# Kernel optimization log

Hardware: AMD Instinct MI355X
Metric: run time of the kernel (lower is better)

## Reference

```python
import jax, jax.numpy as jnp
import numpy as np
from jax import lax

B, T, I, H = 128, 512, 300, 256


def setup_inputs() -> dict:
    key = jax.random.key(0)
    ks = jax.random.split(key, 10)
    k = 1.0 / np.sqrt(H)
    u = lambda kk, shape: jax.random.uniform(kk, shape, jnp.float32, -k, k)
    return {
        "x": jax.random.normal(ks[0], (B, T, I), jnp.float32),
        "W_ih_f": u(ks[1], (4 * H, I)),
        "W_hh_f": u(ks[2], (4 * H, H)),
        "b_f": u(ks[3], (4 * H,)),
        "W_ih_b": u(ks[4], (4 * H, I)),
        "W_hh_b": u(ks[5], (4 * H, H)),
        "b_b": u(ks[6], (4 * H,)),
        "W_lin": u(ks[7], (2, 2 * H)),
        "b_lin": u(ks[8], (2,)),
    }


def _lstm_dir(x, W_ih, W_hh, b, reverse):
    # Precompute input projections for all timesteps: [B, T, 4H]
    xp = jnp.einsum("bti,gi->btg", x, W_ih) + b
    if reverse:
        xp = xp[:, ::-1]
    h0 = jnp.zeros((x.shape[0], H), x.dtype)
    c0 = jnp.zeros((x.shape[0], H), x.dtype)

    def step(carry, xt):
        h, c = carry
        g = xt + h @ W_hh.T  # [B, 4H]
        i_g, f_g, g_g, o_g = jnp.split(g, 4, axis=-1)  # torch gate order i,f,g,o
        i_g = jax.nn.sigmoid(i_g)
        f_g = jax.nn.sigmoid(f_g)
        g_g = jnp.tanh(g_g)
        o_g = jax.nn.sigmoid(o_g)
        c = f_g * c + i_g * g_g
        h = o_g * jnp.tanh(c)
        return (h, c), h

    _, hs = lax.scan(step, (h0, c0), jnp.swapaxes(xp, 0, 1))  # [T, B, H]
    hs = jnp.swapaxes(hs, 0, 1)  # [B, T, H]
    if reverse:
        hs = hs[:, ::-1]
    return hs


def reference(x, W_ih_f, W_hh_f, b_f, W_ih_b, W_hh_b, b_b, W_lin, b_lin):
    hf = _lstm_dir(x, W_ih_f, W_hh_f, b_f, reverse=False)  # [B, T, H]
    hb = _lstm_dir(x, W_ih_b, W_hh_b, b_b, reverse=True)   # [B, T, H]
    last = jnp.concatenate([hf[:, -1], hb[:, -1]], axis=-1)  # [B, 2H]
    return last @ W_lin.T + b_lin  # [B, 2]
```

## Files before the change

### kernel.cpp

```cpp
#include <hip/hip_runtime.h>
#include <cstdint>
#include <cstddef>

typedef _Float16 half2v __attribute__((ext_vector_type(2)));
typedef _Float16 half4v __attribute__((ext_vector_type(4)));
typedef _Float16 half8v __attribute__((ext_vector_type(8)));
typedef float f32x4 __attribute__((ext_vector_type(4)));

#if __has_builtin(__builtin_amdgcn_fdot2)
#define FDOT2(a, b, c) __builtin_amdgcn_fdot2((a), (b), (c), false)
#else
static __device__ __forceinline__ float fdot2_fb(half2v a, half2v b, float c) {
    return c + (float)a[0] * (float)b[0] + (float)a[1] * (float)b[1];
}
#define FDOT2(a, b, c) fdot2_fb((a), (b), (c))
#endif

__device__ __forceinline__ float sigm(float x) { return 1.0f / (1.0f + __expf(-x)); }
__device__ __forceinline__ float tanh_(float x) { return 1.0f - 2.0f / (__expf(2.0f * x) + 1.0f); }

#define BB 128
#define TT 512
#define II 300
#define HH 256
#define GG 1024

__global__ __launch_bounds__(256, 3) void gemm_xp(
    const float* __restrict__ X, const float* __restrict__ W,
    const float* __restrict__ bias, _Float16* __restrict__ XP)
{
    __shared__ _Float16 As[128 * 32];
    __shared__ _Float16 Bs[128 * 32];

    const int t = threadIdx.x;
    const int m0 = blockIdx.y * 128;
    const int n0 = blockIdx.x * 128;
    const int kpos = t & 7;
    const int rbase = t >> 3;
    const int lane = t & 63;
    const int wv = t >> 6;
    const int mq = (wv >> 1) * 4;
    const int nq = (wv & 1) * 4;

    f32x4 acc[4][4];
#pragma unroll
    for (int i = 0; i < 4; ++i)
#pragma unroll
        for (int j = 0; j < 4; ++j) acc[i][j] = f32x4{0.f, 0.f, 0.f, 0.f};

    for (int kc = 0; kc < 320; kc += 32) {
        __syncthreads();
        const int k0 = kc + kpos * 4;
#pragma unroll
        for (int rr = 0; rr < 4; ++rr) {
            const int row = rbase + rr * 32;
            float4 va = {0.f, 0.f, 0.f, 0.f}, vb = {0.f, 0.f, 0.f, 0.f};
            if (k0 < 300) {
                va = *(const float4*)(X + (size_t)(m0 + row) * II + k0);
                vb = *(const float4*)(W + (size_t)(n0 + row) * II + k0);
            }
            const int idx = (row >> 4) * 512 + (kpos >> 1) * 128 + (row & 15) * 8 + (kpos & 1) * 4;
            half4v ha = {(_Float16)va.x, (_Float16)va.y, (_Float16)va.z, (_Float16)va.w};
            half4v hb = {(_Float16)vb.x, (_Float16)vb.y, (_Float16)vb.z, (_Float16)vb.w};
            *(half4v*)(&As[idx]) = ha;
            *(half4v*)(&Bs[idx]) = hb;
        }
        __syncthreads();

        half8v af[4], bf[4];
#pragma unroll
        for (int i = 0; i < 4; ++i) {
            af[i] = *(const half8v*)(&As[(mq + i) * 512 + (lane >> 4) * 128 + (lane & 15) * 8]);
            bf[i] = *(const half8v*)(&Bs[(nq + i) * 512 + (lane >> 4) * 128 + (lane & 15) * 8]);
        }
#pragma unroll
        for (int i = 0; i < 4; ++i)
#pragma unroll
            for (int j = 0; j < 4; ++j)
                acc[i][j] = __builtin_amdgcn_mfma_f32_16x16x32_f16(af[i], bf[j], acc[i][j], 0, 0, 0);
    }

#pragma unroll
    for (int j = 0; j < 4; ++j) {
        const int n = n0 + (nq + j) * 16 + (lane & 15);
        const float bv = bias[n];
#pragma unroll
        for (int i = 0; i < 4; ++i) {
#pragma unroll
            for (int r = 0; r < 4; ++r) {
                const int m = m0 + (mq + i) * 16 + (lane >> 4) * 4 + r;
                XP[(size_t)m * GG + n] = (_Float16)(acc[i][j][r] + bv);
            }
        }
    }
}

__global__ __launch_bounds__(512, 2) void lstm_fwd(
    const float* __restrict__ Whh, const _Float16* __restrict__ XP,
    float* __restrict__ HF)
{
    __shared__ _Float16 wlds[8 * GG * 8];
    __shared__ float glds[GG];
    __shared__ __align__(16) _Float16 hlds[HH];

    const int t = threadIdx.x;
    const int b = blockIdx.x;
    const int r1 = t + 512;

    half2v w0[96], w1[96];
#pragma unroll
    for (int i = 0; i < 48; ++i) {
        float4 v = *(const float4*)(Whh + (size_t)t * HH + i * 4);
        w0[2 * i]     = half2v{(_Float16)v.x, (_Float16)v.y};
        w0[2 * i + 1] = half2v{(_Float16)v.z, (_Float16)v.w};
    }
#pragma unroll
    for (int i = 0; i < 48; ++i) {
        float4 v = *(const float4*)(Whh + (size_t)r1 * HH + i * 4);
        w1[2 * i]     = half2v{(_Float16)v.x, (_Float16)v.y};
        w1[2 * i + 1] = half2v{(_Float16)v.z, (_Float16)v.w};
    }
#pragma unroll
    for (int grp = 0; grp < 8; ++grp) {
        float4 a  = *(const float4*)(Whh + (size_t)t * HH + 192 + grp * 8);
        float4 c4 = *(const float4*)(Whh + (size_t)t * HH + 192 + grp * 8 + 4);
        half8v hv = {(_Float16)a.x, (_Float16)a.y, (_Float16)a.z, (_Float16)a.w,
                     (_Float16)c4.x, (_Float16)c4.y, (_Float16)c4.z, (_Float16)c4.w};
        *(half8v*)(&wlds[grp * (GG * 8) + t * 8]) = hv;
        float4 a2 = *(const float4*)(Whh + (size_t)r1 * HH + 192 + grp * 8);
        float4 c2 = *(const float4*)(Whh + (size_t)r1 * HH + 192 + grp * 8 + 4);
        half8v hv2 = {(_Float16)a2.x, (_Float16)a2.y, (_Float16)a2.z, (_Float16)a2.w,
                      (_Float16)c2.x, (_Float16)c2.y, (_Float16)c2.z, (_Float16)c2.w};
        *(half8v*)(&wlds[grp * (GG * 8) + r1 * 8]) = hv2;
    }
    if (t < HH) hlds[t] = (_Float16)0.f;
    float c = 0.0f;
    __syncthreads();

    const _Float16* xp_b = XP + (size_t)b * TT * GG;
    _Float16 x0 = xp_b[t];
    _Float16 x1 = xp_b[r1];

    for (int ts = 0; ts < TT; ++ts) {
        const _Float16* xp_n = xp_b + ((ts < TT - 1) ? GG : 0);
        const _Float16 nx0 = xp_n[t];
        const _Float16 nx1 = xp_n[r1];

        float a0 = 0.f, a1 = 0.f;
#pragma unroll
        for (int cq = 0; cq < 24; ++cq) {
            half8v hv = *(const half8v*)(&hlds[cq * 8]);
            half2v h0 = __builtin_shufflevector(hv, hv, 0, 1);
            half2v h1 = __builtin_shufflevector(hv, hv, 2, 3);
            half2v h2 = __builtin_shufflevector(hv, hv, 4, 5);
            half2v h3 = __builtin_shufflevector(hv, hv, 6, 7);
            a0 = FDOT2(h0, w0[cq * 4 + 0], a0);
            a1 = FDOT2(h0, w1[cq * 4 + 0], a1);
            a0 = FDOT2(h1, w0[cq * 4 + 1], a0);
            a1 = FDOT2(h1, w1[cq * 4 + 1], a1);
            a0 = FDOT2(h2, w0[cq * 4 + 2], a0);
            a1 = FDOT2(h2, w1[cq * 4 + 2], a1);
            a0 = FDOT2(h3, w0[cq * 4 + 3], a0);
            a1 = FDOT2(h3, w1[cq * 4 + 3], a1);
        }
#define LDS_W_STEP(W_IDX, I0, I1)                                          \
        {                                                                  \
            half2v hp  = __builtin_shufflevector(hv, hv, I0, I1);          \
            half2v wap = __builtin_shufflevector(wa, wa, I0, I1);          \
            half2v wbp = __builtin_shufflevector(wb, wb, I0, I1);          \
            a0 = FDOT2(hp, wap, a0);                                       \
            a1 = FDOT2(hp, wbp, a1);                                       \
        }
#pragma unroll
        for (int grp = 0; grp < 8; ++grp) {
            half8v hv = *(const half8v*)(&hlds[192 + grp * 8]);
            half8v wa = *(const half8v*)(&wlds[grp * (GG * 8) + t * 8]);
            half8v wb = *(const half8v*)(&wlds[grp * (GG * 8) + r1 * 8]);
            LDS_W_STEP(0, 0, 1)
            LDS_W_STEP(1, 2, 3)
            LDS_W_STEP(2, 4, 5)
            LDS_W_STEP(3, 6, 7)
        }
#undef LDS_W_STEP
        const float o0 = a0 + (float)x0;
        const float o1 = a1 + (float)x1;
        glds[t] = o0;
        glds[t + 512] = o1;
        __syncthreads();
        const float p0 = glds[t ^ 256];
        const float p1 = glds[(t ^ 256) + 512];
        const float gi = (t < 256) ? o0 : p0;
        const float gg = (t < 256) ? o1 : p1;
        const float gf = (t < 256) ? p0 : o0;
        const float go = (t < 256) ? p1 : o1;
        c = sigm(gf) * c + sigm(gi) * tanh_(gg);
        const float h = sigm(go) * tanh_(c);
        if (t < HH) {
            hlds[t] = (_Float16)h;
            if (ts == TT - 1) HF[(size_t)b * HH + t] = h;
        }
        __syncthreads();

        x0 = nx0;
        x1 = nx1;
        xp_b = xp_n;
    }
}

__global__ __launch_bounds__(256) void lstm_bwd(
    const float* __restrict__ X, const float* __restrict__ Wih,
    const float* __restrict__ bb, float* __restrict__ HB)
{
    __shared__ float xs[II];
    const int b = blockIdx.x, t = threadIdx.x;
    const float* xrow = X + ((size_t)b * TT + (TT - 1)) * II;
    if (t < 75) *(float4*)(&xs[t * 4]) = *(const float4*)(xrow + t * 4);
    __syncthreads();
    if (t < HH) {
        float ai = 0.f, ag = 0.f, ao = 0.f;
        const float4* wi = (const float4*)(Wih + (size_t)t * II);
        const float4* wg = (const float4*)(Wih + (size_t)(t + 512) * II);
        const float4* wo = (const float4*)(Wih + (size_t)(t + 768) * II);
        for (int k4 = 0; k4 < 75; ++k4) {
            float4 xv = *(const float4*)(&xs[k4 * 4]);
            float4 a = wi[k4], g4 = wg[k4], o4 = wo[k4];
            ai += xv.x * a.x + xv.y * a.y + xv.z * a.z + xv.w * a.w;
            ag += xv.x * g4.x + xv.y * g4.y + xv.z * g4.z + xv.w * g4.w;
            ao += xv.x * o4.x + xv.y * o4.y + xv.z * o4.z + xv.w * o4.w;
        }
        ai += bb[t];
        ag += bb[t + 512];
        ao += bb[t + 768];
        const float cg = sigm(ai) * tanh_(ag);
        HB[(size_t)b * HH + t] = sigm(ao) * tanh_(cg);
    }
}

__global__ __launch_bounds__(256) void final_k(
    const float* __restrict__ HF, const float* __restrict__ HB,
    const float* __restrict__ Wlin, const float* __restrict__ blin,
    float* __restrict__ OUT)
{
    const int t = threadIdx.x;
    const int b = t >> 1, jj = t & 1;
    float acc = blin[jj];
    const float* wf = Wlin + jj * 512;
    const float* wb = Wlin + jj * 512 + 256;
    const float* hf = HF + (size_t)b * HH;
    const float* hb = HB + (size_t)b * HH;
    for (int k = 0; k < HH; k += 4) {
        float4 h4 = *(const float4*)(hf + k);
        float4 w4 = *(const float4*)(wf + k);
        float4 g4 = *(const float4*)(hb + k);
        float4 v4 = *(const float4*)(wb + k);
        acc += h4.x * w4.x + h4.y * w4.y + h4.z * w4.z + h4.w * w4.w;
        acc += g4.x * v4.x + g4.y * v4.y + g4.z * v4.z + g4.w * v4.w;
    }
    OUT[b * 2 + jj] = acc;
}

extern "C" void kernel_launch(void* const* d_in, const int* in_sizes, int n_in,
                              void* d_out, int out_size, void* d_ws, size_t ws_size,
                              hipStream_t stream)
{
    const float* x = (const float*)d_in[0];
    const float* Wihf = (const float*)d_in[1];
    const float* Whhf = (const float*)d_in[2];
    const float* bf = (const float*)d_in[3];
    const float* Wihb = (const float*)d_in[4];
    const float* Whhb = (const float*)d_in[5];
    const float* bbv = (const float*)d_in[6];
    const float* Wlin = (const float*)d_in[7];
    const float* blin = (const float*)d_in[8];
    float* out = (float*)d_out;
    (void)Whhb; (void)in_sizes; (void)n_in; (void)out_size; (void)ws_size;

    _Float16* xp = (_Float16*)d_ws;
    float* hf = (float*)((char*)d_ws + (size_t)BB * TT * GG * 2);
    float* hb = hf + (size_t)BB * HH;

    lstm_bwd<<<BB, 256, 0, stream>>>(x, Wihb, bbv, hb);
    gemm_xp<<<dim3(GG / 128, (BB * TT) / 128), 256, 0, stream>>>(x, Wihf, bf, xp);
    lstm_fwd<<<BB, 512, 0, stream>>>(Whhf, xp, hf);
    final_k<<<1, 256, 0, stream>>>(hf, hb, Wlin, blin, out);
}
```

Before: 1.360 ms.

## Pair gates within a wave via shuffles and double-buffer hidden state

Remaps rows so each wave's two 32-lane halves hold the i/g and f/o gate rows for the same hidden unit. The gates can then be exchanged with __shfl_xor instead of an LDS round trip. The hidden-state buffer is double-buffered, which removes one of the two block-wide barriers per timestep. The cost is a non-contiguous row-to-thread mapping for the LDS weight reads, which may cause bank conflicts, and extra index arithmetic.

```diff
diff --git a/kernel.cpp b/kernel.cpp
--- a/kernel.cpp
+++ b/kernel.cpp
@@ -95,28 +95,33 @@
     }
 }
 
-__global__ __launch_bounds__(512, 2) void lstm_fwd(
+__global__ __attribute__((amdgpu_flat_work_group_size(512, 512), amdgpu_waves_per_eu(2, 2)))
+void lstm_fwd(
     const float* __restrict__ Whh, const _Float16* __restrict__ XP,
     float* __restrict__ HF)
 {
     __shared__ _Float16 wlds[8 * GG * 8];
-    __shared__ float glds[GG];
-    __shared__ __align__(16) _Float16 hlds[HH];
+    __shared__ __align__(16) _Float16 hlds[2][HH];
 
     const int t = threadIdx.x;
     const int b = blockIdx.x;
-    const int r1 = t + 512;
+    const int l = t & 63;
+    const int wv = t >> 6;
+    const int half = l >> 5;
+    const int j = wv * 32 + (l & 31);
+    const int row0 = j + (half ? 256 : 0);
+    const int row1 = row0 + 512;
 
     half2v w0[96], w1[96];
 #pragma unroll
     for (int i = 0; i < 48; ++i) {
-        float4 v = *(const float4*)(Whh + (size_t)t * HH + i * 4);
+        float4 v = *(const float4*)(Whh + (size_t)row0 * HH + i * 4);
         w0[2 * i]     = half2v{(_Float16)v.x, (_Float16)v.y};
         w0[2 * i + 1] = half2v{(_Float16)v.z, (_Float16)v.w};
     }
 #pragma unroll
     for (int i = 0; i < 48; ++i) {
-        float4 v = *(const float4*)(Whh + (size_t)r1 * HH + i * 4);
+        float4 v = *(const float4*)(Whh + (size_t)row1 * HH + i * 4);
         w1[2 * i]     = half2v{(_Float16)v.x, (_Float16)v.y};
         w1[2 * i + 1] = half2v{(_Float16)v.z, (_Float16)v.w};
     }
@@ -127,29 +132,31 @@
         half8v hv = {(_Float16)a.x, (_Float16)a.y, (_Float16)a.z, (_Float16)a.w,
                      (_Float16)c4.x, (_Float16)c4.y, (_Float16)c4.z, (_Float16)c4.w};
         *(half8v*)(&wlds[grp * (GG * 8) + t * 8]) = hv;
-        float4 a2 = *(const float4*)(Whh + (size_t)r1 * HH + 192 + grp * 8);
-        float4 c2 = *(const float4*)(Whh + (size_t)r1 * HH + 192 + grp * 8 + 4);
+        float4 a2 = *(const float4*)(Whh + (size_t)(t + 512) * HH + 192 + grp * 8);
+        float4 c2 = *(const float4*)(Whh + (size_t)(t + 512) * HH + 192 + grp * 8 + 4);
         half8v hv2 = {(_Float16)a2.x, (_Float16)a2.y, (_Float16)a2.z, (_Float16)a2.w,
                       (_Float16)c2.x, (_Float16)c2.y, (_Float16)c2.z, (_Float16)c2.w};
-        *(half8v*)(&wlds[grp * (GG * 8) + r1 * 8]) = hv2;
-    }
-    if (t < HH) hlds[t] = (_Float16)0.f;
+        *(half8v*)(&wlds[grp * (GG * 8) + (t + 512) * 8]) = hv2;
+    }
+    if (t < HH) hlds[0][t] = (_Float16)0.f;
     float c = 0.0f;
     __syncthreads();
 
     const _Float16* xp_b = XP + (size_t)b * TT * GG;
-    _Float16 x0 = xp_b[t];
-    _Float16 x1 = xp_b[r1];
+    _Float16 x0 = xp_b[row0];
+    _Float16 x1 = xp_b[row1];
 
     for (int ts = 0; ts < TT; ++ts) {
+        const int p = ts & 1;
+        const _Float16* hrd = &hlds[p][0];
         const _Float16* xp_n = xp_b + ((ts < TT - 1) ? GG : 0);
-        const _Float16 nx0 = xp_n[t];
-        const _Float16 nx1 = xp_n[r1];
+        const _Float16 nx0 = xp_n[row0];
+        const _Float16 nx1 = xp_n[row1];
 
         float a0 = 0.f, a1 = 0.f;
 #pragma unroll
         for (int cq = 0; cq < 24; ++cq) {
-            half8v hv = *(const half8v*)(&hlds[cq * 8]);
+            half8v hv = *(const half8v*)(&hrd[cq * 8]);
             half2v h0 = __builtin_shufflevector(hv, hv, 0, 1);
             half2v h1 = __builtin_shufflevector(hv, hv, 2, 3);
             half2v h2 = __builtin_shufflevector(hv, hv, 4, 5);
@@ -163,7 +170,7 @@
             a0 = FDOT2(h3, w0[cq * 4 + 3], a0);
             a1 = FDOT2(h3, w1[cq * 4 + 3], a1);
         }
-#define LDS_W_STEP(W_IDX, I0, I1)                                          \
+#define LDS_W_STEP(I0, I1)                                                 \
         {                                                                  \
             half2v hp  = __builtin_shufflevector(hv, hv, I0, I1);          \
             half2v wap = __builtin_shufflevector(wa, wa, I0, I1);          \
@@ -173,31 +180,28 @@
         }
 #pragma unroll
         for (int grp = 0; grp < 8; ++grp) {
-            half8v hv = *(const half8v*)(&hlds[192 + grp * 8]);
-            half8v wa = *(const half8v*)(&wlds[grp * (GG * 8) + t * 8]);
-            half8v wb = *(const half8v*)(&wlds[grp * (GG * 8) + r1 * 8]);
-            LDS_W_STEP(0, 0, 1)
-            LDS_W_STEP(1, 2, 3)
-            LDS_W_STEP(2, 4, 5)
-            LDS_W_STEP(3, 6, 7)
+            half8v hv = *(const half8v*)(&hrd[192 + grp * 8]);
+            half8v wa = *(const half8v*)(&wlds[grp * (GG * 8) + row0 * 8]);
+            half8v wb = *(const half8v*)(&wlds[grp * (GG * 8) + row1 * 8]);
+            LDS_W_STEP(0, 1)
+            LDS_W_STEP(2, 3)
+            LDS_W_STEP(4, 5)
+            LDS_W_STEP(6, 7)
         }
 #undef LDS_W_STEP
         const float o0 = a0 + (float)x0;
         const float o1 = a1 + (float)x1;
-        glds[t] = o0;
-        glds[t + 512] = o1;
-        __syncthreads();
-        const float p0 = glds[t ^ 256];
-        const float p1 = glds[(t ^ 256) + 512];
-        const float gi = (t < 256) ? o0 : p0;
-        const float gg = (t < 256) ? o1 : p1;
-        const float gf = (t < 256) ? p0 : o0;
-        const float go = (t < 256) ? p1 : o1;
+        const float p0 = __shfl_xor(o0, 32, 64);
+        const float p1 = __shfl_xor(o1, 32, 64);
+        const float gi = half ? p0 : o0;
+        const float gg = half ? p1 : o1;
+        const float gf = half ? o0 : p0;
+        const float go = half ? o1 : p1;
         c = sigm(gf) * c + sigm(gi) * tanh_(gg);
         const float h = sigm(go) * tanh_(c);
-        if (t < HH) {
-            hlds[t] = (_Float16)h;
-            if (ts == TT - 1) HF[(size_t)b * HH + t] = h;
+        if (!half) {
+            hlds[p ^ 1][j] = (_Float16)h;
+            if (ts == TT - 1) HF[(size_t)b * HH + j] = h;
         }
         __syncthreads();
 
```

Result: faster. 1.317 ms (-3.1%).
